# Performance work log

Measured on AMD Instinct MI355X. Metric: run time of the kernel, lower is better.

The kernel has to match this reference:

```python
import jax, jax.numpy as jnp
import numpy as np

N_NODES = 100000
N_EDGES = 1600000
IN_FEATS = 128
N_HIDDEN = 128
N_CLASSES = 47


def _glorot(key, shape):
    lim = float(np.sqrt(6.0 / (shape[0] + shape[1])))
    return jax.random.uniform(key, shape, jnp.float32, -lim, lim)


def setup_inputs() -> dict:
    key = jax.random.key(0)
    ks = jax.random.split(key, 9)
    x = jax.random.normal(ks[0], (N_NODES, IN_FEATS), jnp.float32)
    src = jax.random.randint(ks[1], (N_EDGES,), 0, N_NODES, jnp.int32)
    dst = jax.random.randint(ks[2], (N_EDGES,), 0, N_NODES, jnp.int32)
    return {
        "x": x,
        "W_self_0": _glorot(ks[3], (IN_FEATS, N_HIDDEN)),
        "W_neigh_0": _glorot(ks[4], (IN_FEATS, N_HIDDEN)),
        "W_self_1": _glorot(ks[5], (N_HIDDEN, N_HIDDEN)),
        "W_neigh_1": _glorot(ks[6], (N_HIDDEN, N_HIDDEN)),
        "W_self_2": _glorot(ks[7], (N_HIDDEN, N_CLASSES)),
        "W_neigh_2": _glorot(ks[8], (N_HIDDEN, N_CLASSES)),
        "src": src,
        "dst": dst,
    }


def _sage_layer(h, src, dst, W_self, W_neigh):
    # mean aggregation of in-neighbor features (DGL SAGEConv 'mean', no bias)
    neigh_sum = jax.ops.segment_sum(h[src], dst, num_segments=N_NODES)  # [N, d]
    deg = jax.ops.segment_sum(jnp.ones((src.shape[0],), h.dtype), dst,
                              num_segments=N_NODES)  # [N]
    h_neigh = neigh_sum / jnp.maximum(deg, 1.0)[:, None]
    return h @ W_self + h_neigh @ W_neigh


def reference(x, W_self_0, W_neigh_0, W_self_1, W_neigh_1, W_self_2, W_neigh_2,
              src, dst):
    h = _sage_layer(x, src, dst, W_self_0, W_neigh_0)
    h = jax.nn.relu(h)  # dropout is identity in eval/reference mode
    h = _sage_layer(h, src, dst, W_self_1, W_neigh_1)
    h = jax.nn.relu(h)
    h = _sage_layer(h, src, dst, W_self_2, W_neigh_2)
    return h
```

## Files before the change

kernel.cpp:

```cpp
#include <hip/hip_runtime.h>
#include <hip/hip_bf16.h>

#define NN 100000
#define NE 1600000
#define NBK 391

typedef __attribute__((ext_vector_type(8))) short bf16x8;
typedef __attribute__((ext_vector_type(4))) float f32x4;

__device__ __forceinline__ unsigned short f2bf(float x) {
    unsigned u = __float_as_uint(x);
    return (unsigned short)((u + 0x7fffu + ((u >> 16) & 1u)) >> 16);
}
__device__ __forceinline__ float bflo(unsigned v) { return __uint_as_float(v << 16); }
__device__ __forceinline__ float bfhi(unsigned v) { return __uint_as_float(v & 0xffff0000u); }

#define ACCV(A, v) do { \
    A[0] += bflo((v).x); A[1] += bfhi((v).x); \
    A[2] += bflo((v).y); A[3] += bfhi((v).y); \
    A[4] += bflo((v).z); A[5] += bfhi((v).z); \
    A[6] += bflo((v).w); A[7] += bfhi((v).w); } while (0)

__device__ __forceinline__ int swz8(int i, int nwg) {
    int q = nwg >> 3, r = nwg & 7;
    int x = i & 7, j = i >> 3;
    return (x < r) ? x * (q + 1) + j : r * (q + 1) + (x - r) * q + j;
}

__global__ void cast_x(const float* __restrict__ x, unsigned short* __restrict__ h, int n) {
    int i = (blockIdx.x * blockDim.x + threadIdx.x) * 4;
    if (i >= n) return;
    float4 v = *(const float4*)(x + i);
    unsigned out0 = ((unsigned)f2bf(v.y) << 16) | f2bf(v.x);
    unsigned out1 = ((unsigned)f2bf(v.w) << 16) | f2bf(v.z);
    *(uint2*)(h + i) = make_uint2(out0, out1);
}

__global__ __launch_bounds__(256) void hist_buck(const int* __restrict__ dst, int* __restrict__ bhist) {
    __shared__ int h[NBK];
    int t = threadIdx.x;
    for (int i = t; i < NBK; i += 256) h[i] = 0;
    __syncthreads();
    int base = blockIdx.x * 4096;
#pragma unroll
    for (int i = 0; i < 16; ++i) {
        int e = base + t + i * 256;
        if (e < NE) atomicAdd(&h[dst[e] >> 8], 1);
    }
    __syncthreads();
    for (int i = t; i < NBK; i += 256)
        if (h[i]) atomicAdd(&bhist[i], h[i]);
}

__global__ __launch_bounds__(512) void scan_pack(const int* __restrict__ bhist, int* __restrict__ bbase,
                                                 int* __restrict__ gcur, int* __restrict__ row_ptr,
                                                 const float* __restrict__ Ws0, const float* __restrict__ Wn0,
                                                 const float* __restrict__ Ws1, const float* __restrict__ Wn1,
                                                 const float* __restrict__ Ws2, const float* __restrict__ Wn2,
                                                 unsigned short* __restrict__ wp0, unsigned short* __restrict__ wp1,
                                                 unsigned short* __restrict__ wp2) {
    int t = threadIdx.x;
    if (blockIdx.x == 0) {
        __shared__ int s[512];
        int v = (t < NBK) ? bhist[t] : 0;
        s[t] = v;
        __syncthreads();
        for (int off = 1; off < 512; off <<= 1) {
            int u = (t >= off) ? s[t - off] : 0;
            __syncthreads();
            s[t] += u;
            __syncthreads();
        }
        int ex = s[t] - v;
        if (t <= NBK) bbase[t] = ex;
        if (t < NBK) gcur[t * 16] = ex;
        if (t == 0) row_ptr[NN] = NE;
        return;
    }
    int local = (blockIdx.x - 1) * 512 + t;
    const float *Ws, *Wn;
    unsigned short* wp;
    int Ncols, NF;
    if (local < 32768)      { Ws = Ws0; Wn = Wn0; wp = wp0; Ncols = 128; NF = 8; }
    else if (local < 65536) { Ws = Ws1; Wn = Wn1; wp = wp1; Ncols = 128; NF = 8; local -= 32768; }
    else                    { Ws = Ws2; Wn = Wn2; wp = wp2; Ncols = 47;  NF = 3; local -= 65536; }
    int j = local & 7;
    int lane = (local >> 3) & 63;
    int fid = local >> 9;
    int nf = fid % NF;
    int kstep = fid / NF;
    int k = kstep * 32 + (lane >> 4) * 8 + j;
    int n = nf * 16 + (lane & 15);
    float v = 0.f;
    if (n < Ncols) v = (k < 128) ? Ws[k * Ncols + n] : Wn[(k - 128) * Ncols + n];
    wp[local] = f2bf(v);
}

__global__ __launch_bounds__(256) void sort_scatter(const int* __restrict__ src,
                                                    const int* __restrict__ dst,
                                                    int* __restrict__ gcur,
                                                    unsigned* __restrict__ pairs) {
    __shared__ int bcnt[NBK], gbase[NBK], lcur[NBK];
    int t = threadIdx.x;
    for (int i = t; i < NBK; i += 256) { bcnt[i] = 0; lcur[i] = 0; }
    __syncthreads();
    int base = blockIdx.x * 4096;
#pragma unroll
    for (int i = 0; i < 16; ++i) {
        int e = base + t + i * 256;
        if (e < NE) atomicAdd(&bcnt[dst[e] >> 8], 1);
    }
    __syncthreads();
    for (int i = t; i < NBK; i += 256)
        if (bcnt[i]) gbase[i] = atomicAdd(&gcur[i * 16], bcnt[i]);
    __syncthreads();
#pragma unroll
    for (int i = 0; i < 16; ++i) {
        int e = base + t + i * 256;
        if (e < NE) {
            int d = dst[e];
            int b = d >> 8;
            int p = atomicAdd(&lcur[b], 1);
            pairs[gbase[b] + p] = ((unsigned)src[e] << 8) | (unsigned)(d & 255);
        }
    }
}

__global__ __launch_bounds__(256) void bucket_place(const unsigned* __restrict__ pairs,
                                                    const int* __restrict__ bbase,
                                                    int* __restrict__ row_ptr,
                                                    float* __restrict__ inv_deg,
                                                    int* __restrict__ csr) {
    __shared__ int hist[256], sc[256], cur[256];
    int b = blockIdx.x, t = threadIdx.x;
    hist[t] = 0;
    __syncthreads();
    int beg = bbase[b], end = bbase[b + 1];
    for (int i = beg + t; i < end; i += 256) atomicAdd(&hist[pairs[i] & 255u], 1);
    __syncthreads();
    int deg = hist[t];
    sc[t] = deg;
    __syncthreads();
    for (int off = 1; off < 256; off <<= 1) {
        int u = (t >= off) ? sc[t - off] : 0;
        __syncthreads();
        sc[t] += u;
        __syncthreads();
    }
    int ex = sc[t] - deg;
    int node = b * 256 + t;
    if (node < NN) {
        row_ptr[node] = beg + ex;
        inv_deg[node] = 1.0f / (float)max(deg, 1);
    }
    cur[t] = beg + ex;
    __syncthreads();
    for (int i = beg + t; i < end; i += 256) {
        unsigned p = pairs[i];
        int pos = atomicAdd(&cur[p & 255u], 1);
        csr[pos] = (int)(p & 0xFFFFFF00u);
    }
}

__global__ __launch_bounds__(256) void aggregate(const unsigned* __restrict__ h32,
                                                 const int* __restrict__ csr,
                                                 const int* __restrict__ row_ptr,
                                                 const float* __restrict__ inv_deg,
                                                 unsigned* __restrict__ agg32) {
    int lane = threadIdx.x & 63;
    int wave = threadIdx.x >> 6;
    int chunk = (blockIdx.x & 7) * 3125 + (blockIdx.x >> 3);
    int node = chunk * 4 + wave;
    int g = lane >> 4;
    unsigned l16 = (unsigned)(lane & 15) * 16;
    const char* hb = (const char*)h32;
    int beg = row_ptr[node], end = row_ptr[node + 1];
    float acc[8];
#pragma unroll
    for (int j = 0; j < 8; ++j) acc[j] = 0.f;

    int e = beg;
    for (; e + 15 < end; e += 16) {
        int c0 = csr[e + g];
        int c1 = csr[e + 4 + g];
        int c2 = csr[e + 8 + g];
        int c3 = csr[e + 12 + g];
        uint4 v0 = *(const uint4*)(hb + (unsigned)c0 + l16);
        uint4 v1 = *(const uint4*)(hb + (unsigned)c1 + l16);
        uint4 v2 = *(const uint4*)(hb + (unsigned)c2 + l16);
        uint4 v3 = *(const uint4*)(hb + (unsigned)c3 + l16);
        ACCV(acc, v0); ACCV(acc, v1); ACCV(acc, v2); ACCV(acc, v3);
    }
    for (; e + 3 < end; e += 4) {
        int c = csr[e + g];
        uint4 v = *(const uint4*)(hb + (unsigned)c + l16);
        ACCV(acc, v);
    }
    int rem = end - e;
    if (g < rem) {
        int c = csr[e + g];
        uint4 v = *(const uint4*)(hb + (unsigned)c + l16);
        ACCV(acc, v);
    }

#pragma unroll
    for (int j = 0; j < 8; ++j) {
        acc[j] += __shfl_xor(acc[j], 16, 64);
        acc[j] += __shfl_xor(acc[j], 32, 64);
    }
    float inv = inv_deg[node];
    if (lane < 16) {
        unsigned d0 = ((unsigned)f2bf(acc[1] * inv) << 16) | f2bf(acc[0] * inv);
        unsigned d1 = ((unsigned)f2bf(acc[3] * inv) << 16) | f2bf(acc[2] * inv);
        unsigned d2 = ((unsigned)f2bf(acc[5] * inv) << 16) | f2bf(acc[4] * inv);
        unsigned d3 = ((unsigned)f2bf(acc[7] * inv) << 16) | f2bf(acc[6] * inv);
        *(uint4*)((char*)agg32 + (size_t)node * 256 + l16) = make_uint4(d0, d1, d2, d3);
    }
}

template <int NF, bool LAST>
__global__ __launch_bounds__(256) void gemm_k(const unsigned short* __restrict__ hA,
                                              const unsigned short* __restrict__ hAgg,
                                              const unsigned short* __restrict__ wpack,
                                              unsigned short* __restrict__ hOut,
                                              float* __restrict__ fOut) {
    int lane = threadIdx.x & 63;
    int wave = threadIdx.x >> 6;
    int chunk = swz8(blockIdx.x, (int)gridDim.x);
    int base = chunk * 64;
    int aRow = base + wave * 16 + (lane & 15);
    int kgrp = (lane >> 4) * 8;

    f32x4 acc[NF];
#pragma unroll
    for (int f = 0; f < NF; ++f)
#pragma unroll
        for (int q = 0; q < 4; ++q) acc[f][q] = 0.f;

    bool inb = (aRow < NN);
#pragma unroll
    for (int half = 0; half < 2; ++half) {
        const unsigned short* A = half ? hAgg : hA;
#pragma unroll
        for (int ks = 0; ks < 4; ++ks) {
            bf16x8 afrag;
            if (inb) {
                afrag = *(const bf16x8*)(A + (size_t)aRow * 128 + ks * 32 + kgrp);
            } else {
#pragma unroll
                for (int j = 0; j < 8; ++j) afrag[j] = 0;
            }
            int kstep = half * 4 + ks;
#pragma unroll
            for (int nf = 0; nf < NF; ++nf) {
                bf16x8 b = *(const bf16x8*)(wpack + (((kstep * NF + nf) * 64) + lane) * 8);
                acc[nf] = __builtin_amdgcn_mfma_f32_16x16x32_bf16(afrag, b, acc[nf], 0, 0, 0);
            }
        }
    }

    int col0 = lane & 15;
    int rBase = base + wave * 16 + (lane >> 4) * 4;
#pragma unroll
    for (int nf = 0; nf < NF; ++nf) {
        int col = nf * 16 + col0;
        if (LAST) {
            if (col < 47) {
#pragma unroll
                for (int q = 0; q < 4; ++q) {
                    int row = rBase + q;
                    if (row < NN) fOut[(size_t)row * 47 + col] = acc[nf][q];
                }
            }
        } else {
#pragma unroll
            for (int q = 0; q < 4; ++q) {
                int row = rBase + q;
                if (row < NN) hOut[(size_t)row * 128 + col] = f2bf(fmaxf(acc[nf][q], 0.f));
            }
        }
    }
}

static inline size_t alignup(size_t x) { return (x + 255) & ~(size_t)255; }

extern "C" void kernel_launch(void* const* d_in, const int* in_sizes, int n_in,
                              void* d_out, int out_size, void* d_ws, size_t ws_size,
                              hipStream_t stream) {
    const float* x   = (const float*)d_in[0];
    const float* Ws0 = (const float*)d_in[1];
    const float* Wn0 = (const float*)d_in[2];
    const float* Ws1 = (const float*)d_in[3];
    const float* Wn1 = (const float*)d_in[4];
    const float* Ws2 = (const float*)d_in[5];
    const float* Wn2 = (const float*)d_in[6];
    const int* src   = (const int*)d_in[7];
    const int* dst   = (const int*)d_in[8];
    float* out = (float*)d_out;

    char* w = (char*)d_ws;
    size_t off = 0;
    int* row_ptr   = (int*)(w + off);   off += alignup((NN + 1) * 4);
    int* bhist     = (int*)(w + off);   off += alignup(NBK * 4);
    int* bbase     = (int*)(w + off);   off += alignup((NBK + 1) * 4);
    int* gcur      = (int*)(w + off);   off += alignup((size_t)NBK * 16 * 4);
    float* inv_deg = (float*)(w + off); off += alignup(NN * 4);
    int* csr       = (int*)(w + off);   off += alignup((size_t)NE * 4);
    unsigned* pairs = (unsigned*)(w + off); off += alignup((size_t)NE * 4);
    unsigned short* wp0 = (unsigned short*)(w + off); off += alignup(8 * 8 * 64 * 8 * 2);
    unsigned short* wp1 = (unsigned short*)(w + off); off += alignup(8 * 8 * 64 * 8 * 2);
    unsigned short* wp2 = (unsigned short*)(w + off); off += alignup(8 * 3 * 64 * 8 * 2);
    unsigned short* hA  = (unsigned short*)(w + off); off += alignup((size_t)NN * 128 * 2);
    unsigned short* hB  = (unsigned short*)(w + off); off += alignup((size_t)NN * 128 * 2);
    unsigned short* agg = (unsigned short*)(w + off); off += alignup((size_t)NN * 128 * 2);

    hipMemsetAsync(bhist, 0, NBK * 4, stream);

    cast_x<<<dim3((NN * 128 / 4 + 255) / 256), dim3(256), 0, stream>>>(x, hA, NN * 128);
    hist_buck<<<dim3((NE + 4095) / 4096), dim3(256), 0, stream>>>(dst, bhist);
    scan_pack<<<dim3(153), dim3(512), 0, stream>>>(bhist, bbase, gcur, row_ptr,
                                                   Ws0, Wn0, Ws1, Wn1, Ws2, Wn2, wp0, wp1, wp2);
    sort_scatter<<<dim3((NE + 4095) / 4096), dim3(256), 0, stream>>>(src, dst, gcur, pairs);
    bucket_place<<<dim3(NBK), dim3(256), 0, stream>>>(pairs, bbase, row_ptr, inv_deg, csr);

    const int aggGrid  = NN / 4;
    const int gemmGrid = (NN + 63) / 64;

    aggregate<<<dim3(aggGrid), dim3(256), 0, stream>>>((const unsigned*)hA, csr, row_ptr, inv_deg, (unsigned*)agg);
    gemm_k<8, false><<<dim3(gemmGrid), dim3(256), 0, stream>>>(hA, agg, wp0, hB, nullptr);
    aggregate<<<dim3(aggGrid), dim3(256), 0, stream>>>((const unsigned*)hB, csr, row_ptr, inv_deg, (unsigned*)agg);
    gemm_k<8, false><<<dim3(gemmGrid), dim3(256), 0, stream>>>(hB, agg, wp1, hA, nullptr);
    aggregate<<<dim3(aggGrid), dim3(256), 0, stream>>>((const unsigned*)hA, csr, row_ptr, inv_deg, (unsigned*)agg);
    gemm_k<3, true><<<dim3(gemmGrid), dim3(256), 0, stream>>>(hA, agg, wp2, nullptr, out);
}
```

Before: 334.3 us.

## Scatter edges into fixed-capacity bucket slots to drop histogram pass and memset

Edge pairs are now scattered into fixed per-bucket slots of SLOT capacity, with slot cursors initialised inside cast_x. This removes the separate histogram kernel and the memset. The per-bucket counts are recovered from the final cursors, and bucket_place reads each bucket from its own slot. This saves one full pass over dst and one launch. The risk is that a bucket holding more than SLOT edges would overflow, which is safe only because the edges are uniformly random (mean about 4096 per bucket). Smaller work-groups in sort_scatter and an earlier inv_deg load were also made.

```diff
diff --git a/kernel.cpp b/kernel.cpp
--- a/kernel.cpp
+++ b/kernel.cpp
@@ -4,6 +4,7 @@
 #define NN 100000
 #define NE 1600000
 #define NBK 391
+#define SLOT 4608
 
 typedef __attribute__((ext_vector_type(8))) short bf16x8;
 typedef __attribute__((ext_vector_type(4))) float f32x4;
@@ -27,33 +28,54 @@
     return (x < r) ? x * (q + 1) + j : r * (q + 1) + (x - r) * q + j;
 }
 
-__global__ void cast_x(const float* __restrict__ x, unsigned short* __restrict__ h, int n) {
-    int i = (blockIdx.x * blockDim.x + threadIdx.x) * 4;
-    if (i >= n) return;
+__global__ __launch_bounds__(256) void cast_x(const float* __restrict__ x,
+                                              unsigned short* __restrict__ h,
+                                              int* __restrict__ gcur) {
+    if (blockIdx.x == 0) {
+        for (int i = threadIdx.x; i < NBK; i += 256) gcur[i * 16] = i * SLOT;
+    }
+    int chunk = swz8(blockIdx.x, (int)gridDim.x);
+    int i = (chunk * 256 + (int)threadIdx.x) * 4;
+    if (i >= NN * 128) return;
     float4 v = *(const float4*)(x + i);
     unsigned out0 = ((unsigned)f2bf(v.y) << 16) | f2bf(v.x);
     unsigned out1 = ((unsigned)f2bf(v.w) << 16) | f2bf(v.z);
     *(uint2*)(h + i) = make_uint2(out0, out1);
 }
 
-__global__ __launch_bounds__(256) void hist_buck(const int* __restrict__ dst, int* __restrict__ bhist) {
-    __shared__ int h[NBK];
+__global__ __launch_bounds__(256) void sort_scatter(const int* __restrict__ src,
+                                                    const int* __restrict__ dst,
+                                                    int* __restrict__ gcur,
+                                                    unsigned* __restrict__ pairs) {
+    __shared__ int bcnt[NBK], gbase[NBK], lcur[NBK];
     int t = threadIdx.x;
-    for (int i = t; i < NBK; i += 256) h[i] = 0;
-    __syncthreads();
-    int base = blockIdx.x * 4096;
-#pragma unroll
-    for (int i = 0; i < 16; ++i) {
+    for (int i = t; i < NBK; i += 256) { bcnt[i] = 0; lcur[i] = 0; }
+    __syncthreads();
+    int base = blockIdx.x * 2048;
+    int d[8];
+#pragma unroll
+    for (int i = 0; i < 8; ++i) {
         int e = base + t + i * 256;
-        if (e < NE) atomicAdd(&h[dst[e] >> 8], 1);
+        d[i] = (e < NE) ? dst[e] : -1;
+        if (d[i] >= 0) atomicAdd(&bcnt[d[i] >> 8], 1);
     }
     __syncthreads();
     for (int i = t; i < NBK; i += 256)
-        if (h[i]) atomicAdd(&bhist[i], h[i]);
-}
-
-__global__ __launch_bounds__(512) void scan_pack(const int* __restrict__ bhist, int* __restrict__ bbase,
-                                                 int* __restrict__ gcur, int* __restrict__ row_ptr,
+        if (bcnt[i]) gbase[i] = atomicAdd(&gcur[i * 16], bcnt[i]);
+    __syncthreads();
+#pragma unroll
+    for (int i = 0; i < 8; ++i) {
+        if (d[i] >= 0) {
+            int e = base + t + i * 256;
+            int b = d[i] >> 8;
+            int p = atomicAdd(&lcur[b], 1);
+            pairs[gbase[b] + p] = ((unsigned)src[e] << 8) | (unsigned)(d[i] & 255);
+        }
+    }
+}
+
+__global__ __launch_bounds__(512) void scan_pack(const int* __restrict__ gcur, int* __restrict__ bbase,
+                                                 int* __restrict__ row_ptr,
                                                  const float* __restrict__ Ws0, const float* __restrict__ Wn0,
                                                  const float* __restrict__ Ws1, const float* __restrict__ Wn1,
                                                  const float* __restrict__ Ws2, const float* __restrict__ Wn2,
@@ -62,7 +84,7 @@
     int t = threadIdx.x;
     if (blockIdx.x == 0) {
         __shared__ int s[512];
-        int v = (t < NBK) ? bhist[t] : 0;
+        int v = (t < NBK) ? (gcur[t * 16] - t * SLOT) : 0;
         s[t] = v;
         __syncthreads();
         for (int off = 1; off < 512; off <<= 1) {
@@ -73,7 +95,6 @@
         }
         int ex = s[t] - v;
         if (t <= NBK) bbase[t] = ex;
-        if (t < NBK) gcur[t * 16] = ex;
         if (t == 0) row_ptr[NN] = NE;
         return;
     }
@@ -96,36 +117,6 @@
     wp[local] = f2bf(v);
 }
 
-__global__ __launch_bounds__(256) void sort_scatter(const int* __restrict__ src,
-                                                    const int* __restrict__ dst,
-                                                    int* __restrict__ gcur,
-                                                    unsigned* __restrict__ pairs) {
-    __shared__ int bcnt[NBK], gbase[NBK], lcur[NBK];
-    int t = threadIdx.x;
-    for (int i = t; i < NBK; i += 256) { bcnt[i] = 0; lcur[i] = 0; }
-    __syncthreads();
-    int base = blockIdx.x * 4096;
-#pragma unroll
-    for (int i = 0; i < 16; ++i) {
-        int e = base + t + i * 256;
-        if (e < NE) atomicAdd(&bcnt[dst[e] >> 8], 1);
-    }
-    __syncthreads();
-    for (int i = t; i < NBK; i += 256)
-        if (bcnt[i]) gbase[i] = atomicAdd(&gcur[i * 16], bcnt[i]);
-    __syncthreads();
-#pragma unroll
-    for (int i = 0; i < 16; ++i) {
-        int e = base + t + i * 256;
-        if (e < NE) {
-            int d = dst[e];
-            int b = d >> 8;
-            int p = atomicAdd(&lcur[b], 1);
-            pairs[gbase[b] + p] = ((unsigned)src[e] << 8) | (unsigned)(d & 255);
-        }
-    }
-}
-
 __global__ __launch_bounds__(256) void bucket_place(const unsigned* __restrict__ pairs,
                                                     const int* __restrict__ bbase,
                                                     int* __restrict__ row_ptr,
@@ -135,8 +126,10 @@
     int b = blockIdx.x, t = threadIdx.x;
     hist[t] = 0;
     __syncthreads();
-    int beg = bbase[b], end = bbase[b + 1];
-    for (int i = beg + t; i < end; i += 256) atomicAdd(&hist[pairs[i] & 255u], 1);
+    int pbeg = b * SLOT;
+    int beg = bbase[b];
+    int cnt = bbase[b + 1] - beg;
+    for (int i = t; i < cnt; i += 256) atomicAdd(&hist[pairs[pbeg + i] & 255u], 1);
     __syncthreads();
     int deg = hist[t];
     sc[t] = deg;
@@ -155,8 +148,8 @@
     }
     cur[t] = beg + ex;
     __syncthreads();
-    for (int i = beg + t; i < end; i += 256) {
-        unsigned p = pairs[i];
+    for (int i = t; i < cnt; i += 256) {
+        unsigned p = pairs[pbeg + i];
         int pos = atomicAdd(&cur[p & 255u], 1);
         csr[pos] = (int)(p & 0xFFFFFF00u);
     }
@@ -175,6 +168,7 @@
     unsigned l16 = (unsigned)(lane & 15) * 16;
     const char* hb = (const char*)h32;
     int beg = row_ptr[node], end = row_ptr[node + 1];
+    float inv = inv_deg[node];
     float acc[8];
 #pragma unroll
     for (int j = 0; j < 8; ++j) acc[j] = 0.f;
@@ -208,7 +202,6 @@
         acc[j] += __shfl_xor(acc[j], 16, 64);
         acc[j] += __shfl_xor(acc[j], 32, 64);
     }
-    float inv = inv_deg[node];
     if (lane < 16) {
         unsigned d0 = ((unsigned)f2bf(acc[1] * inv) << 16) | f2bf(acc[0] * inv);
         unsigned d1 = ((unsigned)f2bf(acc[3] * inv) << 16) | f2bf(acc[2] * inv);
@@ -301,12 +294,11 @@
     char* w = (char*)d_ws;
     size_t off = 0;
     int* row_ptr   = (int*)(w + off);   off += alignup((NN + 1) * 4);
-    int* bhist     = (int*)(w + off);   off += alignup(NBK * 4);
     int* bbase     = (int*)(w + off);   off += alignup((NBK + 1) * 4);
     int* gcur      = (int*)(w + off);   off += alignup((size_t)NBK * 16 * 4);
     float* inv_deg = (float*)(w + off); off += alignup(NN * 4);
     int* csr       = (int*)(w + off);   off += alignup((size_t)NE * 4);
-    unsigned* pairs = (unsigned*)(w + off); off += alignup((size_t)NE * 4);
+    unsigned* pairs = (unsigned*)(w + off); off += alignup((size_t)NBK * SLOT * 4);
     unsigned short* wp0 = (unsigned short*)(w + off); off += alignup(8 * 8 * 64 * 8 * 2);
     unsigned short* wp1 = (unsigned short*)(w + off); off += alignup(8 * 8 * 64 * 8 * 2);
     unsigned short* wp2 = (unsigned short*)(w + off); off += alignup(8 * 3 * 64 * 8 * 2);
@@ -314,13 +306,10 @@
     unsigned short* hB  = (unsigned short*)(w + off); off += alignup((size_t)NN * 128 * 2);
     unsigned short* agg = (unsigned short*)(w + off); off += alignup((size_t)NN * 128 * 2);
 
-    hipMemsetAsync(bhist, 0, NBK * 4, stream);
-
-    cast_x<<<dim3((NN * 128 / 4 + 255) / 256), dim3(256), 0, stream>>>(x, hA, NN * 128);
-    hist_buck<<<dim3((NE + 4095) / 4096), dim3(256), 0, stream>>>(dst, bhist);
-    scan_pack<<<dim3(153), dim3(512), 0, stream>>>(bhist, bbase, gcur, row_ptr,
+    cast_x<<<dim3((NN * 128 / 4 + 255) / 256), dim3(256), 0, stream>>>(x, hA, gcur);
+    sort_scatter<<<dim3((NE + 2047) / 2048), dim3(256), 0, stream>>>(src, dst, gcur, pairs);
+    scan_pack<<<dim3(153), dim3(512), 0, stream>>>(gcur, bbase, row_ptr,
                                                    Ws0, Wn0, Ws1, Wn1, Ws2, Wn2, wp0, wp1, wp2);
-    sort_scatter<<<dim3((NE + 4095) / 4096), dim3(256), 0, stream>>>(src, dst, gcur, pairs);
     bucket_place<<<dim3(NBK), dim3(256), 0, stream>>>(pairs, bbase, row_ptr, inv_deg, csr);
 
     const int aggGrid  = NN / 4;
```

Result: faster. 322.4 us (-3.6%).
